# Optimization experiments

Hardware: AMD Instinct MI355X
Metric: run time of the kernel (lower is better)

The kernel has to match this reference:

```python
import jax, jax.numpy as jnp
import numpy as np

B, L, D, H = 2, 256, 256, 4
DH = D // H  # 64


def setup_inputs() -> dict:
    key = jax.random.key(0)
    ks = jax.random.split(key, 20)
    inp = {
        "q": jax.random.normal(ks[0], (B, L, D), jnp.float32),
        "k": jax.random.normal(ks[1], (B, L, D), jnp.float32),
        "v": jax.random.normal(ks[2], (B, L, D), jnp.float32),
        "attn_mask": jnp.zeros((L, L), jnp.float32),  # nonzero => masked
        "key_padding_mask": jnp.zeros((B, L), bool),
        "pitch_rel": jax.random.normal(ks[3], (B, L, L, D), jnp.float32),
        "dur_rel": jax.random.normal(ks[4], (B, L, L, D), jnp.float32),
    }
    scale = 1.0 / np.sqrt(D)
    names = ["Wq", "Wk", "Wv", "fc", "pr", "dr"]
    for i, n in enumerate(names):
        inp[n + "_w"] = jax.random.normal(ks[5 + 2 * i], (D, D), jnp.float32) * scale
        inp[n + "_b"] = jax.random.normal(ks[6 + 2 * i], (D,), jnp.float32) * 0.01
    return inp


def _linear(x, w, b):
    # torch nn.Linear: y = x @ W^T + b
    return jnp.matmul(x, w.T) + b


def reference(q, k, v, attn_mask, key_padding_mask, pitch_rel, dur_rel,
              Wq_w, Wq_b, Wk_w, Wk_b, Wv_w, Wv_b, fc_w, fc_b,
              pr_w, pr_b, dr_w, dr_b):
    Bq, Lq, Dm = q.shape
    Lk = k.shape[1]
    # project and split heads -> (B, H, L, DH)
    def heads(x, w, b):
        return _linear(x, w, b).reshape(Bq, -1, H, DH).transpose(0, 2, 1, 3)
    qh, kh, vh = heads(q, Wq_w, Wq_b), heads(k, Wk_w, Wk_b), heads(v, Wv_w, Wv_b)

    # content scores: (B, H, Lq, Lk)
    logits = jnp.einsum("bhid,bhjd->bhij", qh, kh)

    # relative pitch bias: pitch_rel (B, Lq, Lk, D) -> (B, Lq, Lk, H, DH)
    pr = _linear(pitch_rel, pr_w, pr_b).reshape(Bq, Lq, Lk, H, DH)
    logits = logits + jnp.einsum("bhid,bijhd->bhij", qh, pr)

    dr = _linear(dur_rel, dr_w, dr_b).reshape(Bq, Lq, Lk, H, DH)
    logits = logits + jnp.einsum("bhid,bijhd->bhij", qh, dr)

    logits = logits / np.sqrt(DH)

    # mask: key_padding_mask broadcast over the QUERY axis (as in source),
    # attn_mask nonzero => masked
    mask = jnp.logical_or(key_padding_mask[:, None, :, None],
                          (attn_mask != 0)[None, None, :, :])
    logits = jnp.where(mask, jnp.float32(-9e15), logits)

    attn = jax.nn.softmax(logits, axis=-1)  # (B, H, Lq, Lk)
    out = jnp.einsum("bhij,bhjd->bhid", attn, vh)  # (B, H, Lq, DH)
    out = out.transpose(0, 2, 1, 3).reshape(Bq, Lq, Dm)
    out = _linear(out, fc_w, fc_b)  # dropout is identity in eval mode
    return out, attn
```

## Files before the change

kernel.cpp:

```cpp
#include <hip/hip_runtime.h>
#include <math.h>


typedef float f4v __attribute__((ext_vector_type(4)));

#define SLD(dst, ptr)                                                     \
  asm volatile("global_load_dwordx4 %0, %1, off sc0 sc1 nt"               \
               : "=v"(dst)                                                \
               : "v"((unsigned long long)(const void*)(ptr))              \
               : "memory")

#define VW(n)                                             \
  asm volatile("s_waitcnt vmcnt(%0)" ::"i"(n) : "memory"); \
  __builtin_amdgcn_sched_barrier(0)

__global__ __launch_bounds__(256) void k_proj(
    const float* __restrict__ q, const float* __restrict__ k_, const float* __restrict__ v,
    const float* __restrict__ Wq, const float* __restrict__ Bq,
    const float* __restrict__ Wk, const float* __restrict__ Bk,
    const float* __restrict__ Wv, const float* __restrict__ Bv,
    float* __restrict__ qh, float* __restrict__ kh, float* __restrict__ vh) {
  int blk = blockIdx.x;
  int m = blk >> 5;
  int r = blk & 31;
  int b = r >> 4, it = (r >> 2) & 3, ot = r & 3;
  const float* X = (m == 0) ? q : (m == 1) ? k_ : v;
  const float* W = (m == 0) ? Wq : (m == 1) ? Wk : Wv;
  const float* Bs = (m == 0) ? Bq : (m == 1) ? Bk : Bv;
  float* OUT = (m == 0) ? qh : (m == 1) ? kh : vh;
  const float scale = (m == 0) ? 0.125f : 1.0f;

  __shared__ float xs[64][33];
  __shared__ float ws[64][33];
  int tid = threadIdx.x;
  int ti = tid >> 4, to = tid & 15;
  int lr = tid >> 2, lc = (tid & 3) * 8;
  float acc[4][4] = {};

  for (int k0 = 0; k0 < 256; k0 += 32) {
    float4 a0 = *(const float4*)(X + (size_t)(b * 256 + it * 64 + lr) * 256 + k0 + lc);
    float4 a1 = *(const float4*)(X + (size_t)(b * 256 + it * 64 + lr) * 256 + k0 + lc + 4);
    xs[lr][lc + 0] = a0.x; xs[lr][lc + 1] = a0.y; xs[lr][lc + 2] = a0.z; xs[lr][lc + 3] = a0.w;
    xs[lr][lc + 4] = a1.x; xs[lr][lc + 5] = a1.y; xs[lr][lc + 6] = a1.z; xs[lr][lc + 7] = a1.w;
    float4 w0 = *(const float4*)(W + (size_t)(ot * 64 + lr) * 256 + k0 + lc);
    float4 w1 = *(const float4*)(W + (size_t)(ot * 64 + lr) * 256 + k0 + lc + 4);
    ws[lr][lc + 0] = w0.x; ws[lr][lc + 1] = w0.y; ws[lr][lc + 2] = w0.z; ws[lr][lc + 3] = w0.w;
    ws[lr][lc + 4] = w1.x; ws[lr][lc + 5] = w1.y; ws[lr][lc + 6] = w1.z; ws[lr][lc + 7] = w1.w;
    __syncthreads();
#pragma unroll
    for (int kk = 0; kk < 32; ++kk) {
      float xv0 = xs[ti * 4 + 0][kk], xv1 = xs[ti * 4 + 1][kk];
      float xv2 = xs[ti * 4 + 2][kk], xv3 = xs[ti * 4 + 3][kk];
      float wv0 = ws[0 * 16 + to][kk], wv1 = ws[1 * 16 + to][kk];
      float wv2 = ws[2 * 16 + to][kk], wv3 = ws[3 * 16 + to][kk];
      acc[0][0] += xv0 * wv0; acc[0][1] += xv0 * wv1; acc[0][2] += xv0 * wv2; acc[0][3] += xv0 * wv3;
      acc[1][0] += xv1 * wv0; acc[1][1] += xv1 * wv1; acc[1][2] += xv1 * wv2; acc[1][3] += xv1 * wv3;
      acc[2][0] += xv2 * wv0; acc[2][1] += xv2 * wv1; acc[2][2] += xv2 * wv2; acc[2][3] += xv2 * wv3;
      acc[3][0] += xv3 * wv0; acc[3][1] += xv3 * wv1; acc[3][2] += xv3 * wv2; acc[3][3] += xv3 * wv3;
    }
    __syncthreads();
  }
#pragma unroll
  for (int ii = 0; ii < 4; ++ii)
#pragma unroll
    for (int oo = 0; oo < 4; ++oo) {
      int i = it * 64 + ti * 4 + ii;
      int dd = oo * 16 + to;
      OUT[(size_t)((b * 4 + ot) * 256 + i) * 64 + dd] = (acc[ii][oo] + Bs[ot * 64 + dd]) * scale;
    }
}

static __device__ void body_qprdr(int blk, const float* __restrict__ qh,
                                  const float* __restrict__ prw, const float* __restrict__ drw,
                                  float* __restrict__ qpr, float* __restrict__ qdr) {
  int t = blk >> 7;
  int r2 = blk & 127;
  int rt = r2 >> 2, et = r2 & 3;
  const float* W = t ? drw : prw;
  float* OUT = t ? qdr : qpr;
  int h = (rt >> 2) & 3;

  __shared__ float xs[64][33];
  __shared__ float ws2[32][64];
  int tid = threadIdx.x;
  int ti = tid >> 4, to = tid & 15;
  float acc[4][4] = {};

  for (int k0 = 0; k0 < 64; k0 += 32) {
    int lr = tid >> 2, lc = (tid & 3) * 8;
    float4 a0 = *(const float4*)(qh + (size_t)(rt * 64 + lr) * 64 + k0 + lc);
    float4 a1 = *(const float4*)(qh + (size_t)(rt * 64 + lr) * 64 + k0 + lc + 4);
    xs[lr][lc + 0] = a0.x; xs[lr][lc + 1] = a0.y; xs[lr][lc + 2] = a0.z; xs[lr][lc + 3] = a0.w;
    xs[lr][lc + 4] = a1.x; xs[lr][lc + 5] = a1.y; xs[lr][lc + 6] = a1.z; xs[lr][lc + 7] = a1.w;
    int wr = tid >> 3, wc = (tid & 7) * 8;
    float4 w0 = *(const float4*)(W + (size_t)(h * 64 + k0 + wr) * 256 + et * 64 + wc);
    float4 w1 = *(const float4*)(W + (size_t)(h * 64 + k0 + wr) * 256 + et * 64 + wc + 4);
    ws2[wr][wc + 0] = w0.x; ws2[wr][wc + 1] = w0.y; ws2[wr][wc + 2] = w0.z; ws2[wr][wc + 3] = w0.w;
    ws2[wr][wc + 4] = w1.x; ws2[wr][wc + 5] = w1.y; ws2[wr][wc + 6] = w1.z; ws2[wr][wc + 7] = w1.w;
    __syncthreads();
#pragma unroll
    for (int kk = 0; kk < 32; ++kk) {
      float xv0 = xs[ti * 4 + 0][kk], xv1 = xs[ti * 4 + 1][kk];
      float xv2 = xs[ti * 4 + 2][kk], xv3 = xs[ti * 4 + 3][kk];
      float wv0 = ws2[kk][0 * 16 + to], wv1 = ws2[kk][1 * 16 + to];
      float wv2 = ws2[kk][2 * 16 + to], wv3 = ws2[kk][3 * 16 + to];
      acc[0][0] += xv0 * wv0; acc[0][1] += xv0 * wv1; acc[0][2] += xv0 * wv2; acc[0][3] += xv0 * wv3;
      acc[1][0] += xv1 * wv0; acc[1][1] += xv1 * wv1; acc[1][2] += xv1 * wv2; acc[1][3] += xv1 * wv3;
      acc[2][0] += xv2 * wv0; acc[2][1] += xv2 * wv1; acc[2][2] += xv2 * wv2; acc[2][3] += xv2 * wv3;
      acc[3][0] += xv3 * wv0; acc[3][1] += xv3 * wv1; acc[3][2] += xv3 * wv2; acc[3][3] += xv3 * wv3;
    }
    __syncthreads();
  }
#pragma unroll
  for (int ii = 0; ii < 4; ++ii)
#pragma unroll
    for (int oo = 0; oo < 4; ++oo)
      OUT[(size_t)(rt * 64 + ti * 4 + ii) * 256 + et * 64 + oo * 16 + to] = acc[ii][oo];
}

static __device__ void body_qk(int blk, const float* __restrict__ qh,
                               const float* __restrict__ kh, float* __restrict__ qk) {
  int bh = blk >> 4, it = (blk >> 2) & 3, jt = blk & 3;
  __shared__ float xs[64][33];
  __shared__ float ys[64][33];
  int tid = threadIdx.x;
  int ti = tid >> 4, to = tid & 15;
  float acc[4][4] = {};

  for (int k0 = 0; k0 < 64; k0 += 32) {
    int lr = tid >> 2, lc = (tid & 3) * 8;
    float4 a0 = *(const float4*)(qh + (size_t)(bh * 256 + it * 64 + lr) * 64 + k0 + lc);
    float4 a1 = *(const float4*)(qh + (size_t)(bh * 256 + it * 64 + lr) * 64 + k0 + lc + 4);
    xs[lr][lc + 0] = a0.x; xs[lr][lc + 1] = a0.y; xs[lr][lc + 2] = a0.z; xs[lr][lc + 3] = a0.w;
    xs[lr][lc + 4] = a1.x; xs[lr][lc + 5] = a1.y; xs[lr][lc + 6] = a1.z; xs[lr][lc + 7] = a1.w;
    float4 b0 = *(const float4*)(kh + (size_t)(bh * 256 + jt * 64 + lr) * 64 + k0 + lc);
    float4 b1 = *(const float4*)(kh + (size_t)(bh * 256 + jt * 64 + lr) * 64 + k0 + lc + 4);
    ys[lr][lc + 0] = b0.x; ys[lr][lc + 1] = b0.y; ys[lr][lc + 2] = b0.z; ys[lr][lc + 3] = b0.w;
    ys[lr][lc + 4] = b1.x; ys[lr][lc + 5] = b1.y; ys[lr][lc + 6] = b1.z; ys[lr][lc + 7] = b1.w;
    __syncthreads();
#pragma unroll
    for (int kk = 0; kk < 32; ++kk) {
      float xv0 = xs[ti * 4 + 0][kk], xv1 = xs[ti * 4 + 1][kk];
      float xv2 = xs[ti * 4 + 2][kk], xv3 = xs[ti * 4 + 3][kk];
      float wv0 = ys[0 * 16 + to][kk], wv1 = ys[1 * 16 + to][kk];
      float wv2 = ys[2 * 16 + to][kk], wv3 = ys[3 * 16 + to][kk];
      acc[0][0] += xv0 * wv0; acc[0][1] += xv0 * wv1; acc[0][2] += xv0 * wv2; acc[0][3] += xv0 * wv3;
      acc[1][0] += xv1 * wv0; acc[1][1] += xv1 * wv1; acc[1][2] += xv1 * wv2; acc[1][3] += xv1 * wv3;
      acc[2][0] += xv2 * wv0; acc[2][1] += xv2 * wv1; acc[2][2] += xv2 * wv2; acc[2][3] += xv2 * wv3;
      acc[3][0] += xv3 * wv0; acc[3][1] += xv3 * wv1; acc[3][2] += xv3 * wv2; acc[3][3] += xv3 * wv3;
    }
    __syncthreads();
  }
#pragma unroll
  for (int ii = 0; ii < 4; ++ii)
#pragma unroll
    for (int jj = 0; jj < 4; ++jj)
      qk[(size_t)(bh * 256 + it * 64 + ti * 4 + ii) * 256 + jt * 64 + jj * 16 + to] = acc[ii][jj];
}

static __device__ void body_transpose(int blk, const float* __restrict__ in,
                                      float* __restrict__ out) {
  __shared__ float t[32][33];
  int bx = blk & 7, by = blk >> 3;
  int x = threadIdx.x & 31, y0 = threadIdx.x >> 5;
#pragma unroll
  for (int yy = 0; yy < 32; yy += 8)
    t[yy + y0][x] = in[(size_t)(by * 32 + yy + y0) * 256 + bx * 32 + x];
  __syncthreads();
#pragma unroll
  for (int yy = 0; yy < 32; yy += 8)
    out[(size_t)(bx * 32 + yy + y0) * 256 + by * 32 + x] = t[x][yy + y0];
}

__global__ __launch_bounds__(256) void k_mid(
    const float* __restrict__ qh, const float* __restrict__ kh,
    const float* __restrict__ prw, const float* __restrict__ drw,
    float* __restrict__ qpr, float* __restrict__ qdr, float* __restrict__ qk,
    const float* __restrict__ fcw, float* __restrict__ fcT) {
  int blk = blockIdx.x;
  if (blk < 256) body_qprdr(blk, qh, prw, drw, qpr, qdr);
  else if (blk < 384) body_qk(blk - 256, qh, kh, qk);
  else body_transpose(blk - 384, fcw, fcT);
}

__global__ __launch_bounds__(256, 4) void k_bias(
    const float* __restrict__ pitch, const float* __restrict__ dur,
    const float* __restrict__ qpr, const float* __restrict__ qdr,
    float* __restrict__ bias) {
  int blk = blockIdx.x;
  int jc = blk & 3;
  int bi = blk >> 2;
  int b = bi >> 8, i = bi & 255;
  int tid = threadIdx.x, w = tid >> 6, l = tid & 63;
  int j0 = jc * 64 + w * 16;

  __shared__ float red[4][4][4][65];

  float4 qp[4], qd[4];
#pragma unroll
  for (int h = 0; h < 4; ++h) {
    qp[h] = *(const float4*)(qpr + (size_t)((b * 4 + h) * 256 + i) * 256 + 4 * l);
    qd[h] = *(const float4*)(qdr + (size_t)((b * 4 + h) * 256 + i) * 256 + 4 * l);
  }

  int p2 = l & 15, row_o = p2 >> 2, h_o = p2 & 3, sub = l >> 4;
  size_t obase = ((size_t)(b * 4 + h_o) * 256 + i) * 256 + j0 + row_o;

  const float* pbase = pitch + ((size_t)bi * 256 + j0) * 256 + 4 * l;
  const float* dbase = dur + ((size_t)bi * 256 + j0) * 256 + 4 * l;

  asm volatile("s_waitcnt vmcnt(0)" ::: "memory");

  f4v PA[4], DA[4], PB[4], DB[4];

#define ISSUE(PP, DD, g)                                  \
  {                                                       \
    _Pragma("unroll") for (int r = 0; r < 4; ++r) {       \
      SLD(PP[r], pbase + ((g) * 4 + r) * 256);            \
      SLD(DD[r], dbase + ((g) * 4 + r) * 256);            \
    }                                                     \
  }

#define COMPUTE(PP, DD, g)                                                        \
  {                                                                               \
    _Pragma("unroll") for (int r = 0; r < 4; ++r) {                               \
      red[w][r][0][l] = PP[r].x * qp[0].x + PP[r].y * qp[0].y + PP[r].z * qp[0].z \
                      + PP[r].w * qp[0].w + DD[r].x * qd[0].x + DD[r].y * qd[0].y \
                      + DD[r].z * qd[0].z + DD[r].w * qd[0].w;                    \
      red[w][r][1][l] = PP[r].x * qp[1].x + PP[r].y * qp[1].y + PP[r].z * qp[1].z \
                      + PP[r].w * qp[1].w + DD[r].x * qd[1].x + DD[r].y * qd[1].y \
                      + DD[r].z * qd[1].z + DD[r].w * qd[1].w;                    \
      red[w][r][2][l] = PP[r].x * qp[2].x + PP[r].y * qp[2].y + PP[r].z * qp[2].z \
                      + PP[r].w * qp[2].w + DD[r].x * qd[2].x + DD[r].y * qd[2].y \
                      + DD[r].z * qd[2].z + DD[r].w * qd[2].w;                    \
      red[w][r][3][l] = PP[r].x * qp[3].x + PP[r].y * qp[3].y + PP[r].z * qp[3].z \
                      + PP[r].w * qp[3].w + DD[r].x * qd[3].x + DD[r].y * qd[3].y \
                      + DD[r].z * qd[3].z + DD[r].w * qd[3].w;                    \
    }                                                                             \
    float x = 0.f;                                                                \
    {                                                                             \
      const float* rr = &red[w][row_o][h_o][sub * 16];                            \
      _Pragma("unroll") for (int c = 0; c < 16; ++c) x += rr[c];                  \
    }                                                                             \
    x += __shfl_xor(x, 16);                                                       \
    x += __shfl_xor(x, 32);                                                       \
    if (l < 16) bias[obase + (g) * 4] = x;                                        \
  }

  ISSUE(PA, DA, 0);
  ISSUE(PB, DB, 1);
  VW(8);
  COMPUTE(PA, DA, 0);
  ISSUE(PA, DA, 2);
  VW(8);
  COMPUTE(PB, DB, 1);
  ISSUE(PB, DB, 3);
  VW(8);
  COMPUTE(PA, DA, 2);
  VW(0);
  COMPUTE(PB, DB, 3);
#undef ISSUE
#undef COMPUTE
}

__global__ __launch_bounds__(256) void k_pvfc(
    const float* __restrict__ bias, const float* __restrict__ amask,
    const unsigned char* __restrict__ kpm, const float* __restrict__ vh,
    const float* __restrict__ fcT, const float* __restrict__ fcb,
    float* __restrict__ attn, float* __restrict__ out) {
  int b = blockIdx.x >> 8, i = blockIdx.x & 255;
  int tid = threadIdx.x;
  int h = tid >> 6, l = tid & 63;

  __shared__ float arow[4][256];
  __shared__ float pre[256];

  bool rowm = kpm[b * 256 + i] != 0;
  float* qrow = attn + (size_t)((b * 4 + h) * 256 + i) * 256;
  const float* brow = bias + (size_t)((b * 4 + h) * 256 + i) * 256;
  float4 v4 = *(float4*)(qrow + 4 * l);
  float4 b4 = *(const float4*)(brow + 4 * l);
  float4 m4 = *(const float4*)(amask + (size_t)i * 256 + 4 * l);
  float v0 = (rowm || m4.x != 0.f) ? -9e15f : v4.x + b4.x;
  float v1 = (rowm || m4.y != 0.f) ? -9e15f : v4.y + b4.y;
  float v2 = (rowm || m4.z != 0.f) ? -9e15f : v4.z + b4.z;
  float v3 = (rowm || m4.w != 0.f) ? -9e15f : v4.w + b4.w;

  float mx = fmaxf(fmaxf(v0, v1), fmaxf(v2, v3));
#pragma unroll
  for (int m = 1; m <= 32; m <<= 1) mx = fmaxf(mx, __shfl_xor(mx, m));
  float e0 = __expf(v0 - mx), e1 = __expf(v1 - mx);
  float e2 = __expf(v2 - mx), e3 = __expf(v3 - mx);
  float sm = e0 + e1 + e2 + e3;
#pragma unroll
  for (int m = 1; m <= 32; m <<= 1) sm += __shfl_xor(sm, m);
  float inv = 1.0f / sm;
  float4 a4 = make_float4(e0 * inv, e1 * inv, e2 * inv, e3 * inv);
  *(float4*)(qrow + 4 * l) = a4;
  *(float4*)&arow[h][4 * l] = a4;

  float acc = 0.f;
  const float* vbase = vh + (size_t)(b * 4 + h) * 256 * 64 + l;
#pragma unroll 4
  for (int jj = 0; jj < 256; ++jj) acc += arow[h][jj] * vbase[(size_t)jj * 64];
  pre[tid] = acc;
  __syncthreads();

  float acc2 = fcb[tid];
#pragma unroll 4
  for (int c = 0; c < 256; ++c) acc2 += pre[c] * fcT[(size_t)c * 256 + tid];
  out[(size_t)(b * 256 + i) * 256 + tid] = acc2;
}

extern "C" void kernel_launch(void* const* d_in, const int* in_sizes, int n_in,
                              void* d_out, int out_size, void* d_ws, size_t ws_size,
                              hipStream_t stream) {
  (void)in_sizes; (void)n_in; (void)out_size; (void)ws_size;
  const float* q = (const float*)d_in[0];
  const float* k = (const float*)d_in[1];
  const float* v = (const float*)d_in[2];
  const float* amask = (const float*)d_in[3];
  const unsigned char* kpm = (const unsigned char*)d_in[4];
  const float* pitch = (const float*)d_in[5];
  const float* dur = (const float*)d_in[6];
  const float* Wq = (const float*)d_in[7];
  const float* Bq = (const float*)d_in[8];
  const float* Wk = (const float*)d_in[9];
  const float* Bk = (const float*)d_in[10];
  const float* Wv = (const float*)d_in[11];
  const float* Bv = (const float*)d_in[12];
  const float* fcw = (const float*)d_in[13];
  const float* fcb = (const float*)d_in[14];
  const float* prw = (const float*)d_in[15];
  const float* drw = (const float*)d_in[17];

  float* out = (float*)d_out;
  float* attn = out + 2 * 256 * 256;

  float* wsf = (float*)d_ws;
  float* qh = wsf;
  float* kh = qh + 131072;
  float* vh = kh + 131072;
  float* qpr = vh + 131072;
  float* qdr = qpr + 524288;
  float* fcT = qdr + 524288;
  float* bias = fcT + 65536;

  k_proj<<<96, 256, 0, stream>>>(q, k, v, Wq, Bq, Wk, Bk, Wv, Bv, qh, kh, vh);
  k_mid<<<448, 256, 0, stream>>>(qh, kh, prw, drw, qpr, qdr, attn, fcw, fcT);
  k_bias<<<2048, 256, 0, stream>>>(pitch, dur, qpr, qdr, bias);
  k_pvfc<<<512, 256, 0, stream>>>(bias, amask, kpm, vh, fcT, fcb, attn, out);
}
```

Measured before the change: 114.0 us.

## Fuse relative-bias reduction with softmax, PV and output projection kernel

```diff
diff --git a/kernel.cpp b/kernel.cpp
--- a/kernel.cpp
+++ b/kernel.cpp
@@ -183,18 +183,21 @@
   else body_transpose(blk - 384, fcw, fcT);
 }
 
-__global__ __launch_bounds__(256, 4) void k_bias(
+__global__ __launch_bounds__(256, 4) void k_fused3(
     const float* __restrict__ pitch, const float* __restrict__ dur,
     const float* __restrict__ qpr, const float* __restrict__ qdr,
-    float* __restrict__ bias) {
-  int blk = blockIdx.x;
-  int jc = blk & 3;
-  int bi = blk >> 2;
+    const float* __restrict__ amask, const unsigned char* __restrict__ kpm,
+    const float* __restrict__ vh, const float* __restrict__ fcT,
+    const float* __restrict__ fcb, float* __restrict__ attn,
+    float* __restrict__ out) {
+  int bi = blockIdx.x;
   int b = bi >> 8, i = bi & 255;
   int tid = threadIdx.x, w = tid >> 6, l = tid & 63;
-  int j0 = jc * 64 + w * 16;
+  int j0 = w * 64;
 
   __shared__ float red[4][4][4][65];
+  __shared__ float logits[4][264];
+  __shared__ float pre[256];
 
   float4 qp[4], qd[4];
 #pragma unroll
@@ -203,8 +206,12 @@
     qd[h] = *(const float4*)(qdr + (size_t)((b * 4 + h) * 256 + i) * 256 + 4 * l);
   }
 
+  float* qrow = attn + (size_t)((b * 4 + w) * 256 + i) * 256;
+  float4 qk4 = *(const float4*)(qrow + 4 * l);
+  float4 m4 = *(const float4*)(amask + (size_t)i * 256 + 4 * l);
+  bool rowm = kpm[b * 256 + i] != 0;
+
   int p2 = l & 15, row_o = p2 >> 2, h_o = p2 & 3, sub = l >> 4;
-  size_t obase = ((size_t)(b * 4 + h_o) * 256 + i) * 256 + j0 + row_o;
 
   const float* pbase = pitch + ((size_t)bi * 256 + j0) * 256 + 4 * l;
   const float* dbase = dur + ((size_t)bi * 256 + j0) * 256 + 4 * l;
@@ -244,47 +251,34 @@
     }                                                                             \
     x += __shfl_xor(x, 16);                                                       \
     x += __shfl_xor(x, 32);                                                       \
-    if (l < 16) bias[obase + (g) * 4] = x;                                        \
+    if (l < 16) logits[h_o][j0 + (g) * 4 + row_o] = x;                            \
   }
 
   ISSUE(PA, DA, 0);
   ISSUE(PB, DB, 1);
-  VW(8);
-  COMPUTE(PA, DA, 0);
-  ISSUE(PA, DA, 2);
-  VW(8);
-  COMPUTE(PB, DB, 1);
-  ISSUE(PB, DB, 3);
-  VW(8);
-  COMPUTE(PA, DA, 2);
-  VW(0);
-  COMPUTE(PB, DB, 3);
+#pragma unroll
+  for (int gg = 0; gg < 8; ++gg) {
+    VW(8);
+    COMPUTE(PA, DA, 2 * gg);
+    if (gg < 7) ISSUE(PA, DA, 2 * gg + 2);
+    if (gg < 7) {
+      VW(8);
+    } else {
+      VW(0);
+    }
+    COMPUTE(PB, DB, 2 * gg + 1);
+    if (gg < 7) ISSUE(PB, DB, 2 * gg + 3);
+  }
 #undef ISSUE
 #undef COMPUTE
-}
-
-__global__ __launch_bounds__(256) void k_pvfc(
-    const float* __restrict__ bias, const float* __restrict__ amask,
-    const unsigned char* __restrict__ kpm, const float* __restrict__ vh,
-    const float* __restrict__ fcT, const float* __restrict__ fcb,
-    float* __restrict__ attn, float* __restrict__ out) {
-  int b = blockIdx.x >> 8, i = blockIdx.x & 255;
-  int tid = threadIdx.x;
-  int h = tid >> 6, l = tid & 63;
-
-  __shared__ float arow[4][256];
-  __shared__ float pre[256];
-
-  bool rowm = kpm[b * 256 + i] != 0;
-  float* qrow = attn + (size_t)((b * 4 + h) * 256 + i) * 256;
-  const float* brow = bias + (size_t)((b * 4 + h) * 256 + i) * 256;
-  float4 v4 = *(float4*)(qrow + 4 * l);
-  float4 b4 = *(const float4*)(brow + 4 * l);
-  float4 m4 = *(const float4*)(amask + (size_t)i * 256 + 4 * l);
-  float v0 = (rowm || m4.x != 0.f) ? -9e15f : v4.x + b4.x;
-  float v1 = (rowm || m4.y != 0.f) ? -9e15f : v4.y + b4.y;
-  float v2 = (rowm || m4.z != 0.f) ? -9e15f : v4.z + b4.z;
-  float v3 = (rowm || m4.w != 0.f) ? -9e15f : v4.w + b4.w;
+  __syncthreads();
+
+  float* lrow = &logits[w][0];
+  float4 bv = *(float4*)(lrow + 4 * l);
+  float v0 = (rowm || m4.x != 0.f) ? -9e15f : qk4.x + bv.x;
+  float v1 = (rowm || m4.y != 0.f) ? -9e15f : qk4.y + bv.y;
+  float v2 = (rowm || m4.z != 0.f) ? -9e15f : qk4.z + bv.z;
+  float v3 = (rowm || m4.w != 0.f) ? -9e15f : qk4.w + bv.w;
 
   float mx = fmaxf(fmaxf(v0, v1), fmaxf(v2, v3));
 #pragma unroll
@@ -297,12 +291,12 @@
   float inv = 1.0f / sm;
   float4 a4 = make_float4(e0 * inv, e1 * inv, e2 * inv, e3 * inv);
   *(float4*)(qrow + 4 * l) = a4;
-  *(float4*)&arow[h][4 * l] = a4;
+  *(float4*)(lrow + 4 * l) = a4;
 
   float acc = 0.f;
-  const float* vbase = vh + (size_t)(b * 4 + h) * 256 * 64 + l;
+  const float* vbase = vh + (size_t)(b * 4 + w) * 256 * 64 + l;
 #pragma unroll 4
-  for (int jj = 0; jj < 256; ++jj) acc += arow[h][jj] * vbase[(size_t)jj * 64];
+  for (int jj = 0; jj < 256; ++jj) acc += lrow[jj] * vbase[(size_t)jj * 64];
   pre[tid] = acc;
   __syncthreads();
 
@@ -344,10 +338,8 @@
   float* qpr = vh + 131072;
   float* qdr = qpr + 524288;
   float* fcT = qdr + 524288;
-  float* bias = fcT + 65536;
 
   k_proj<<<96, 256, 0, stream>>>(q, k, v, Wq, Bq, Wk, Bk, Wv, Bv, qh, kh, vh);
   k_mid<<<448, 256, 0, stream>>>(qh, kh, prw, drw, qpr, qdr, attn, fcw, fcT);
-  k_bias<<<2048, 256, 0, stream>>>(pitch, dur, qpr, qdr, bias);
-  k_pvfc<<<512, 256, 0, stream>>>(bias, amask, kpm, vh, fcT, fcb, attn, out);
-}
+  k_fused3<<<512, 256, 0, stream>>>(pitch, dur, qpr, qdr, amask, kpm, vh, fcT, fcb, attn, out);
+}
```

Measured after the change: 108.1 us. 5.1% less time.
